# Kernel optimization log

Hardware: AMD Instinct MI355X
Metric: run time of the kernel (lower is better)

Reference implementation:

```python
import jax, jax.numpy as jnp
import numpy as np

V, D, T, L, H = 32000, 1024, 2048, 2, 16
HS = D // H  # per-head dim (head_size // nheads)
FF = 4 * D
EPS = 1e-5


def _ln(x, g, b):
    m = jnp.mean(x, axis=-1, keepdims=True)
    v = jnp.mean((x - m) ** 2, axis=-1, keepdims=True)
    return (x - m) * jax.lax.rsqrt(v + EPS) * g + b


def setup_inputs() -> dict:
    key = jax.random.key(0)
    ks = jax.random.split(key, 16)
    s = lambda k, shape, fan: jax.random.normal(k, shape, jnp.float32) * (fan ** -0.5)
    return {
        "inputs": jax.random.randint(ks[0], (1, T), 0, V, dtype=jnp.int64),
        "tok_emb": s(ks[1], (V, D), D),
        "pos_emb": s(ks[2], (T, D), D),
        "ln1_g": jnp.ones((L, D)), "ln1_b": jnp.zeros((L, D)),
        "wq": s(ks[3], (L, H, D, HS), D),
        "wk": s(ks[4], (L, H, D, HS), D),
        "wv": s(ks[5], (L, H, D, HS), D),
        "ln2_g": jnp.ones((L, D)), "ln2_b": jnp.zeros((L, D)),
        "w1": s(ks[6], (L, D, FF), D), "b1": jnp.zeros((L, FF)),
        "w2": s(ks[7], (L, FF, D), FF), "b2": jnp.zeros((L, D)),
        "lnf_g": jnp.ones((D,)), "lnf_b": jnp.zeros((D,)),
        "w_un": s(ks[8], (D, V), D), "b_un": jnp.zeros((V,)),
    }


def reference(inputs, tok_emb, pos_emb, ln1_g, ln1_b, wq, wk, wv,
              ln2_g, ln2_b, w1, b1, w2, b2, lnf_g, lnf_b, w_un, b_un):
    b, t = inputs.shape
    x = tok_emb[inputs] + pos_emb[:t]  # [B,T,D]
    mask = jnp.tril(jnp.ones((t, t), dtype=bool))
    scale = jnp.asarray(D, x.dtype) ** -0.5  # source scales by x.shape[-1]**-0.5
    neg_inf = jnp.asarray(-jnp.inf, x.dtype)
    for l in range(L):
        h = _ln(x, ln1_g[l], ln1_b[l])
        q = jnp.einsum('btc,hcs->bhts', h, wq[l])
        k = jnp.einsum('btc,hcs->bhts', h, wk[l])
        v = jnp.einsum('btc,hcs->bhts', h, wv[l])
        scores = jnp.einsum('bhts,bhus->bhtu', q, k) * scale  # [B,H,T,T]
        scores = jnp.where(mask, scores, neg_inf)
        p = jax.nn.softmax(scores, axis=-1)
        att = jnp.einsum('bhtu,bhus->bhts', p, v)  # [B,H,T,HS]
        att = att.transpose(0, 2, 1, 3).reshape(b, t, H * HS)
        x = x + att
        h = _ln(x, ln2_g[l], ln2_b[l])
        h = jax.nn.relu(h @ w1[l] + b1[l]) @ w2[l] + b2[l]
        x = x + h
    x = _ln(x, lnf_g, lnf_b)
    return x @ w_un + b_un  # [B,T,V]
```

## Files before the change

### kernel.cpp

```cpp
#include <hip/hip_runtime.h>
#include <hip/hip_bf16.h>

#define TT 2048
#define DD 1024
#define NH 16
#define HSZ 64
#define FFD 4096
#define VV 32000
#define NL 2

typedef __bf16 bf16x8 __attribute__((ext_vector_type(8)));
typedef float f32x4 __attribute__((ext_vector_type(4)));

__device__ __forceinline__ unsigned short f2bf(float f) {
    unsigned int u = __float_as_uint(f);
    return (unsigned short)((u + 0x7FFFu + ((u >> 16) & 1u)) >> 16);
}

#define GLL(gsrc, ldst) \
  __builtin_amdgcn_global_load_lds((const __attribute__((address_space(1))) void*)(gsrc), \
                                   (__attribute__((address_space(3))) void*)(ldst), 16, 0, 0)

#define SWZ64(L)  ((L) ^ ((((L) >> 7) & 3) << 4))
#define SWZ128(L) ((L) ^ ((((L) >> 7) & 7) << 4))

__global__ __launch_bounds__(256) void embed_kernel(
    const int* __restrict__ idx, const float* __restrict__ tok,
    const float* __restrict__ pos, float* __restrict__ x)
{
    int t = blockIdx.x;
    int d4 = threadIdx.x * 4;
    int token = idx[t];
    float4 a = *(const float4*)&tok[(size_t)token * DD + d4];
    float4 p = *(const float4*)&pos[(size_t)t * DD + d4];
    float4 r;
    r.x = a.x + p.x; r.y = a.y + p.y; r.z = a.z + p.z; r.w = a.w + p.w;
    *(float4*)&x[(size_t)t * DD + d4] = r;
}

__global__ __launch_bounds__(256) void ln_kernel(
    const float* __restrict__ x, const float* __restrict__ g,
    const float* __restrict__ b, unsigned short* __restrict__ out)
{
    int t = blockIdx.x;
    int tid = threadIdx.x;
    int d4 = tid * 4;
    float4 xv = *(const float4*)&x[(size_t)t * DD + d4];
    float s  = xv.x + xv.y + xv.z + xv.w;
    float s2 = xv.x*xv.x + xv.y*xv.y + xv.z*xv.z + xv.w*xv.w;
    #pragma unroll
    for (int off = 32; off >= 1; off >>= 1) {
        s  += __shfl_xor(s,  off);
        s2 += __shfl_xor(s2, off);
    }
    __shared__ float ls[4], ls2[4];
    int w = tid >> 6;
    if ((tid & 63) == 0) { ls[w] = s; ls2[w] = s2; }
    __syncthreads();
    float sum  = ls[0] + ls[1] + ls[2] + ls[3];
    float sum2 = ls2[0] + ls2[1] + ls2[2] + ls2[3];
    float mean = sum * (1.0f / DD);
    float var  = sum2 * (1.0f / DD) - mean * mean;
    float r = rsqrtf(var + 1e-5f);
    float4 gv = *(const float4*)&g[d4];
    float4 bv = *(const float4*)&b[d4];
    ushort4 pk;
    pk.x = f2bf((xv.x - mean) * r * gv.x + bv.x);
    pk.y = f2bf((xv.y - mean) * r * gv.y + bv.y);
    pk.z = f2bf((xv.z - mean) * r * gv.z + bv.z);
    pk.w = f2bf((xv.w - mean) * r * gv.w + bv.w);
    *(ushort4*)&out[(size_t)t * DD + d4] = pk;
}

__global__ __launch_bounds__(256) void tcast(
    const float* __restrict__ src, unsigned short* __restrict__ dst,
    int R, int C, size_t sstride, size_t dstride)
{
    __shared__ float tile[64][65];
    const float* s = src + (size_t)blockIdx.z * sstride;
    unsigned short* d = dst + (size_t)blockIdx.z * dstride;
    int c0 = blockIdx.x * 64, r0 = blockIdx.y * 64;
    #pragma unroll
    for (int i = 0; i < 16; ++i) {
        int id = i * 256 + threadIdx.x;
        int rr = id >> 6, cc = id & 63;
        tile[rr][cc] = s[(size_t)(r0 + rr) * C + (c0 + cc)];
    }
    __syncthreads();
    #pragma unroll
    for (int i = 0; i < 16; ++i) {
        int id = i * 256 + threadIdx.x;
        int cc = id >> 6, rr = id & 63;
        d[(size_t)(c0 + cc) * R + (r0 + rr)] = f2bf(tile[rr][cc]);
    }
}

__global__ __launch_bounds__(256) void qkv_tcast(
    const float* __restrict__ wq, const float* __restrict__ wk,
    const float* __restrict__ wv, unsigned short* __restrict__ dst)
{
    __shared__ float tile[64][65];
    int l = blockIdx.z;
    int mat = blockIdx.y >> 4, hh = blockIdx.y & 15;
    const float* s = (mat == 0) ? wq : (mat == 1) ? wk : wv;
    s += (((size_t)l * NH + hh) * DD) * HSZ;
    int r0 = blockIdx.x * 64;
    #pragma unroll
    for (int i = 0; i < 16; ++i) {
        int id = i * 256 + threadIdx.x;
        int rr = id >> 6, cc = id & 63;
        tile[rr][cc] = s[(size_t)(r0 + rr) * HSZ + cc];
    }
    __syncthreads();
    unsigned short* d = dst + (size_t)l * 3072 * DD + ((size_t)mat * DD + hh * HSZ) * DD;
    #pragma unroll
    for (int i = 0; i < 16; ++i) {
        int id = i * 256 + threadIdx.x;
        int cc = id >> 6, rr = id & 63;
        d[(size_t)cc * DD + (r0 + rr)] = f2bf(tile[rr][cc]);
    }
}

template<int EPI>
__global__ __launch_bounds__(256) void mgemm(
    const unsigned short* __restrict__ A, const unsigned short* __restrict__ Bt,
    const float* __restrict__ bias, void* __restrict__ outp,
    int M, int N, int K)
{
    __shared__ unsigned short As[3][128 * 32];
    __shared__ unsigned short Bs[3][128 * 32];
    int tid = threadIdx.x;
    int w = tid >> 6, lane = tid & 63;
    int l15 = lane & 15, l4 = lane >> 4;
    int bm = blockIdx.y * 128, bn = blockIdx.x * 128;
    int wr = (w >> 1) * 64, wc = (w & 1) * 64;

    f32x4 zz = {0.f, 0.f, 0.f, 0.f};
    f32x4 acc[4][4];
    #pragma unroll
    for (int m = 0; m < 4; ++m)
        #pragma unroll
        for (int n = 0; n < 4; ++n) acc[m][n] = zz;

    int t16 = tid * 16;
    int lg = SWZ64(t16);
    int srow = lg >> 6;
    int skel = (lg & 63) >> 1;
    const unsigned short* aS0 = A + (size_t)(bm + srow) * K + skel;
    const unsigned short* aS1 = A + (size_t)(bm + 64 + srow) * K + skel;
    const unsigned short* bS0 = Bt + (size_t)(bn + srow) * K + skel;
    const unsigned short* bS1 = Bt + (size_t)(bn + 64 + srow) * K + skel;

    #define STAGE(t, slot) do { int kk_ = (t) * 32; \
        GLL(aS0 + kk_, (char*)As[slot] + w * 1024); \
        GLL(aS1 + kk_, (char*)As[slot] + 4096 + w * 1024); \
        GLL(bS0 + kk_, (char*)Bs[slot] + w * 1024); \
        GLL(bS1 + kk_, (char*)Bs[slot] + 4096 + w * 1024); } while (0)

    int aoff[4], boff[4];
    #pragma unroll
    for (int m = 0; m < 4; ++m) {
        int la = (wr + m * 16 + l15) * 64 + l4 * 16;
        aoff[m] = SWZ64(la);
        int lb = (wc + m * 16 + l15) * 64 + l4 * 16;
        boff[m] = SWZ64(lb);
    }

    int nt = K >> 5;
    STAGE(0, 0);
    STAGE(1, 1);
    STAGE(2, 2);
    int slot = 0;
    for (int t = 0; t < nt; ++t) {
        if (t + 2 < nt)      asm volatile("s_waitcnt vmcnt(8)" ::: "memory");
        else if (t + 1 < nt) asm volatile("s_waitcnt vmcnt(4)" ::: "memory");
        else                 asm volatile("s_waitcnt vmcnt(0)" ::: "memory");
        __builtin_amdgcn_sched_barrier(0);
        __builtin_amdgcn_s_barrier();
        __builtin_amdgcn_sched_barrier(0);
        bf16x8 af[4], bfr[4];
        #pragma unroll
        for (int m = 0; m < 4; ++m) af[m] = *(const bf16x8*)((const char*)As[slot] + aoff[m]);
        #pragma unroll
        for (int n = 0; n < 4; ++n) bfr[n] = *(const bf16x8*)((const char*)Bs[slot] + boff[n]);
        #pragma unroll
        for (int m = 0; m < 4; ++m)
            #pragma unroll
            for (int n = 0; n < 4; ++n)
                acc[m][n] = __builtin_amdgcn_mfma_f32_16x16x32_bf16(af[m], bfr[n], acc[m][n], 0, 0, 0);
        __builtin_amdgcn_sched_barrier(0);
        __builtin_amdgcn_s_barrier();
        __builtin_amdgcn_sched_barrier(0);
        if (t + 3 < nt) STAGE(t + 3, slot);
        slot = (slot == 2) ? 0 : slot + 1;
    }
    #undef STAGE

    #pragma unroll
    for (int m = 0; m < 4; ++m) {
        int row0 = bm + wr + m * 16 + l4 * 4;
        #pragma unroll
        for (int n = 0; n < 4; ++n) {
            int col = bn + wc + n * 16 + l15;
            f32x4 v = acc[m][n];
            if (EPI == 0) {
                int mat = col >> 10, hh = (col >> 6) & 15, ss = col & 63;
                unsigned short* base = (unsigned short*)outp + (size_t)mat * ((size_t)NH * TT * HSZ);
                if (mat < 2) {
                    #pragma unroll
                    for (int i = 0; i < 4; ++i)
                        base[((size_t)hh * TT + row0 + i) * HSZ + ss] = f2bf(v[i]);
                } else {
                    ushort4 pk;
                    pk.x = f2bf(v[0]); pk.y = f2bf(v[1]); pk.z = f2bf(v[2]); pk.w = f2bf(v[3]);
                    *(ushort4*)&base[((size_t)hh * HSZ + ss) * TT + row0] = pk;
                }
            } else if (EPI == 1) {
                float bb = bias[col];
                unsigned short* o = (unsigned short*)outp;
                #pragma unroll
                for (int i = 0; i < 4; ++i)
                    o[(size_t)(row0 + i) * FFD + col] = f2bf(fmaxf(v[i] + bb, 0.f));
            } else if (EPI == 2) {
                float bb = bias[col];
                float* xx = (float*)outp;
                #pragma unroll
                for (int i = 0; i < 4; ++i)
                    xx[(size_t)(row0 + i) * DD + col] += v[i] + bb;
            }
        }
    }
}

__global__ __launch_bounds__(512, 2) void mgemm256(
    const unsigned short* __restrict__ A, const unsigned short* __restrict__ Bt,
    const float* __restrict__ bias, float* __restrict__ outp,
    int M, int N, int K)
{
    __shared__ unsigned short As[3][2][128 * 32];
    __shared__ unsigned short Bs[3][2][128 * 32];
    int tid = threadIdx.x;
    int w = tid >> 6, lane = tid & 63;
    int l15 = lane & 15, l4 = lane >> 4;
    int wr = w >> 2, wc = w & 3;
    int bid = blockIdx.x;
    int xcd = bid & 7, j = bid >> 3;
    int mt = j & 7, p = xcd * 16 + (j >> 3);
    if (p >= N / 256) return;
    int bm = mt * 256, bn = p * 256;

    f32x4 zz = {0.f, 0.f, 0.f, 0.f};
    f32x4 acc[8][4];
    #pragma unroll
    for (int m = 0; m < 8; ++m)
        #pragma unroll
        for (int n = 0; n < 4; ++n) acc[m][n] = zz;

    int L0 = tid * 16;
    int Ls = SWZ64(L0);
    int srow = Ls >> 6;
    int skel = (Ls & 63) >> 1;
    const unsigned short* aS[2], *bS[2];
    aS[0] = A + (size_t)(bm + srow) * K + skel;
    aS[1] = A + (size_t)(bm + 128 + srow) * K + skel;
    bS[0] = Bt + (size_t)(bn + srow) * K + skel;
    bS[1] = Bt + (size_t)(bn + 128 + srow) * K + skel;

    #define STAGE6(t, slot) do { int kk_ = (t) * 32; \
        GLL(aS[0] + kk_, (char*)As[slot][0] + w * 1024); \
        GLL(aS[1] + kk_, (char*)As[slot][1] + w * 1024); \
        GLL(bS[0] + kk_, (char*)Bs[slot][0] + w * 1024); \
        GLL(bS[1] + kk_, (char*)Bs[slot][1] + w * 1024); } while (0)

    int aoff[8], boff[4];
    #pragma unroll
    for (int m = 0; m < 8; ++m)
        aoff[m] = SWZ64((m * 16 + l15) * 64 + l4 * 16);
    #pragma unroll
    for (int n = 0; n < 4; ++n)
        boff[n] = SWZ64(((wc & 1) * 64 + n * 16 + l15) * 64 + l4 * 16);

    int nt = K >> 5;
    STAGE6(0, 0);
    STAGE6(1, 1);
    STAGE6(2, 2);
    int slot = 0;
    for (int t = 0; t < nt; ++t) {
        if (t + 2 < nt)      asm volatile("s_waitcnt vmcnt(8)" ::: "memory");
        else if (t + 1 < nt) asm volatile("s_waitcnt vmcnt(4)" ::: "memory");
        else                 asm volatile("s_waitcnt vmcnt(0)" ::: "memory");
        __builtin_amdgcn_sched_barrier(0);
        __builtin_amdgcn_s_barrier();
        __builtin_amdgcn_sched_barrier(0);
        const char* ab = (const char*)As[slot][wr];
        const char* bb = (const char*)Bs[slot][wc >> 1];
        bf16x8 bfr[4];
        #pragma unroll
        for (int n = 0; n < 4; ++n) bfr[n] = *(const bf16x8*)(bb + boff[n]);
        __builtin_amdgcn_s_setprio(1);
        #pragma unroll
        for (int m = 0; m < 8; ++m) {
            bf16x8 af = *(const bf16x8*)(ab + aoff[m]);
            #pragma unroll
            for (int n = 0; n < 4; ++n)
                acc[m][n] = __builtin_amdgcn_mfma_f32_16x16x32_bf16(af, bfr[n], acc[m][n], 0, 0, 0);
        }
        __builtin_amdgcn_s_setprio(0);
        __builtin_amdgcn_sched_barrier(0);
        __builtin_amdgcn_s_barrier();
        __builtin_amdgcn_sched_barrier(0);
        if (t + 3 < nt) STAGE6(t + 3, slot);
        slot = (slot == 2) ? 0 : slot + 1;
    }
    #undef STAGE6

    #pragma unroll
    for (int m = 0; m < 8; ++m) {
        int row0 = bm + wr * 128 + m * 16 + l4 * 4;
        #pragma unroll
        for (int n = 0; n < 4; ++n) {
            int col = bn + wc * 64 + n * 16 + l15;
            float bb = bias[col];
            f32x4 v = acc[m][n];
            #pragma unroll
            for (int i = 0; i < 4; ++i)
                outp[(size_t)(row0 + i) * VV + col] = v[i] + bb;
        }
    }
}

__global__ __launch_bounds__(256) void attn_kernel(
    const unsigned short* __restrict__ qg, const unsigned short* __restrict__ kg,
    const unsigned short* __restrict__ vt, float* __restrict__ x)
{
    __shared__ unsigned short Ks[2][64 * 64];
    __shared__ unsigned short Vs[2][64 * 64];
    __shared__ unsigned short Ps[4][16 * 64];
    int tid = threadIdx.x;
    int w = tid >> 6, lane = tid & 63;
    int l15 = lane & 15, l4 = lane >> 4;
    int hh = blockIdx.y;
    int qb = (31 - blockIdx.x) * 64;

    const unsigned short* qrow = qg + ((size_t)hh * TT + qb + w * 16 + l15) * HSZ + l4 * 8;
    bf16x8 qf0 = *(const bf16x8*)(qrow);
    bf16x8 qf1 = *(const bf16x8*)(qrow + 32);

    int t16 = tid * 16;
    int lgs = SWZ128(t16);
    int surow = lgs >> 7;
    int subyte = lgs & 127;
    const char* kbase = (const char*)(kg + (size_t)hh * TT * HSZ);
    const char* vbase = (const char*)(vt + (size_t)hh * HSZ * TT);

    #define ASTAGE(ib, buf) do { \
        int ub_ = (ib) * 64; \
        GLL(kbase + (size_t)(ub_ + surow) * 128 + subyte,          (char*)Ks[buf] + w * 1024); \
        GLL(kbase + (size_t)(ub_ + 32 + surow) * 128 + subyte,     (char*)Ks[buf] + 4096 + w * 1024); \
        GLL(vbase + (size_t)surow * 4096 + ub_ * 2 + subyte,       (char*)Vs[buf] + w * 1024); \
        GLL(vbase + (size_t)(surow + 32) * 4096 + ub_ * 2 + subyte,(char*)Vs[buf] + 4096 + w * 1024); \
    } while (0)

    f32x4 zz = {0.f, 0.f, 0.f, 0.f};
    f32x4 o[4];
    #pragma unroll
    for (int i = 0; i < 4; ++i) o[i] = zz;
    float mrun = -INFINITY, lrun = 0.f;

    const float scale = 0.03125f;
    int nkv = (qb >> 6) + 1;
    ASTAGE(0, 0);
    if (nkv > 1) ASTAGE(1, 1);
    int cur = 0;
    for (int ib = 0; ib < nkv; ++ib) {
        bool diag = (ib * 64 == qb);
        if (ib + 1 < nkv) asm volatile("s_waitcnt vmcnt(4)" ::: "memory");
        else              asm volatile("s_waitcnt vmcnt(0)" ::: "memory");
        __builtin_amdgcn_sched_barrier(0);
        __builtin_amdgcn_s_barrier();
        __builtin_amdgcn_sched_barrier(0);
        const char* ksc = (const char*)Ks[cur];
        const char* vsc = (const char*)Vs[cur];

        f32x4 sfr[4];
        __builtin_amdgcn_s_setprio(1);
        #pragma unroll
        for (int f = 0; f < 4; ++f) {
            int lgb = (f * 16 + l15) * 128 + l4 * 16;
            bf16x8 k0 = *(const bf16x8*)(ksc + SWZ128(lgb));
            bf16x8 k1 = *(const bf16x8*)(ksc + SWZ128(lgb + 64));
            f32x4 z = zz;
            z = __builtin_amdgcn_mfma_f32_16x16x32_bf16(k0, qf0, z, 0, 0, 0);
            z = __builtin_amdgcn_mfma_f32_16x16x32_bf16(k1, qf1, z, 0, 0, 0);
            sfr[f] = z;
        }
        __builtin_amdgcn_s_setprio(0);

        float mx = -INFINITY;
        #pragma unroll
        for (int f = 0; f < 4; ++f)
            #pragma unroll
            for (int i = 0; i < 4; ++i) {
                float s = sfr[f][i] * scale;
                if (diag && (16 * f + (l4 << 2) + i) > (w * 16 + l15)) s = -INFINITY;
                sfr[f][i] = s;
                mx = fmaxf(mx, s);
            }
        mx = fmaxf(mx, __shfl_xor(mx, 16));
        mx = fmaxf(mx, __shfl_xor(mx, 32));
        bool grow = __any(mx > mrun + 8.0f);
        float c = 1.0f;
        if (grow) {
            float mn = fmaxf(mrun, mx);
            c = __expf(mrun - mn);
            mrun = mn;
        }
        float ps = 0.f;
        #pragma unroll
        for (int f = 0; f < 4; ++f)
            #pragma unroll
            for (int i = 0; i < 4; ++i) {
                float p = __expf(sfr[f][i] - mrun);
                sfr[f][i] = p;
                ps += p;
            }
        ps += __shfl_xor(ps, 16);
        ps += __shfl_xor(ps, 32);
        lrun = lrun * c + ps;
        if (grow) {
            #pragma unroll
            for (int i = 0; i < 4; ++i) {
                float ci = __shfl(c, (lane & 48) + (l4 << 2) + i);
                #pragma unroll
                for (int sf = 0; sf < 4; ++sf) o[sf][i] *= ci;
            }
        }

        unsigned short* pw = Ps[w];
        #pragma unroll
        for (int f = 0; f < 4; ++f) {
            unsigned a0 = ((unsigned)f2bf(sfr[f][0])) | (((unsigned)f2bf(sfr[f][1])) << 16);
            unsigned a1 = ((unsigned)f2bf(sfr[f][2])) | (((unsigned)f2bf(sfr[f][3])) << 16);
            int byte0 = l15 * 128 + (16 * f + (l4 << 2)) * 2;
            *(unsigned*)((char*)pw + SWZ128(byte0)) = a0;
            *(unsigned*)((char*)pw + SWZ128(byte0 + 4)) = a1;
        }
        bf16x8 pa0 = *(const bf16x8*)((const char*)pw + SWZ128(l15 * 128 + l4 * 16));
        bf16x8 pa1 = *(const bf16x8*)((const char*)pw + SWZ128(l15 * 128 + 64 + l4 * 16));
        __builtin_amdgcn_s_setprio(1);
        #pragma unroll
        for (int sf = 0; sf < 4; ++sf) {
            int lgb = (sf * 16 + l15) * 128 + l4 * 16;
            bf16x8 v0 = *(const bf16x8*)(vsc + SWZ128(lgb));
            bf16x8 v1 = *(const bf16x8*)(vsc + SWZ128(lgb + 64));
            o[sf] = __builtin_amdgcn_mfma_f32_16x16x32_bf16(pa0, v0, o[sf], 0, 0, 0);
            o[sf] = __builtin_amdgcn_mfma_f32_16x16x32_bf16(pa1, v1, o[sf], 0, 0, 0);
        }
        __builtin_amdgcn_s_setprio(0);
        __builtin_amdgcn_sched_barrier(0);
        __builtin_amdgcn_s_barrier();
        __builtin_amdgcn_sched_barrier(0);
        if (ib + 2 < nkv) ASTAGE(ib + 2, cur);
        cur ^= 1;
    }
    #undef ASTAGE
    float rl[4];
    #pragma unroll
    for (int i = 0; i < 4; ++i)
        rl[i] = 1.0f / __shfl(lrun, (lane & 48) + (l4 << 2) + i);
    #pragma unroll
    for (int sf = 0; sf < 4; ++sf)
        #pragma unroll
        for (int i = 0; i < 4; ++i) {
            int q = qb + w * 16 + l4 * 4 + i;
            int d = hh * HSZ + sf * 16 + l15;
            x[(size_t)q * DD + d] += o[sf][i] * rl[i];
        }
}

extern "C" void kernel_launch(void* const* d_in, const int* in_sizes, int n_in,
                              void* d_out, int out_size, void* d_ws, size_t ws_size,
                              hipStream_t stream)
{
    const int*   idx    = (const int*)  d_in[0];
    const float* tok    = (const float*)d_in[1];
    const float* pos    = (const float*)d_in[2];
    const float* ln1_g  = (const float*)d_in[3];
    const float* ln1_b  = (const float*)d_in[4];
    const float* wq     = (const float*)d_in[5];
    const float* wk     = (const float*)d_in[6];
    const float* wv     = (const float*)d_in[7];
    const float* ln2_g  = (const float*)d_in[8];
    const float* ln2_b  = (const float*)d_in[9];
    const float* w1     = (const float*)d_in[10];
    const float* b1     = (const float*)d_in[11];
    const float* w2     = (const float*)d_in[12];
    const float* b2     = (const float*)d_in[13];
    const float* lnf_g  = (const float*)d_in[14];
    const float* lnf_b  = (const float*)d_in[15];
    const float* w_un   = (const float*)d_in[16];
    const float* b_un   = (const float*)d_in[17];
    float* out = (float*)d_out;

    char* W = (char*)d_ws;
    float*          x    = (float*)(W);
    unsigned short* h    = (unsigned short*)(W + 8388608);
    unsigned short* qg   = (unsigned short*)(W + 12582912);
    unsigned short* kg   = (unsigned short*)(W + 16777216);
    unsigned short* vt   = (unsigned short*)(W + 20971520);
    unsigned short* h1   = (unsigned short*)(W + 25165824);
    unsigned short* wqkvT= (unsigned short*)(W + 41943040);
    unsigned short* w1T  = (unsigned short*)(W + 54525952);
    unsigned short* w2T  = (unsigned short*)(W + 71303168);
    unsigned short* wunT = (unsigned short*)(W + 88080384);
    (void)kg; (void)ws_size; (void)in_sizes; (void)n_in; (void)out_size;

    qkv_tcast<<<dim3(16, 48, 2), 256, 0, stream>>>(wq, wk, wv, wqkvT);
    tcast<<<dim3(64, 16, 2), 256, 0, stream>>>(w1, w1T, DD, FFD, (size_t)DD * FFD, (size_t)DD * FFD);
    tcast<<<dim3(16, 64, 2), 256, 0, stream>>>(w2, w2T, FFD, DD, (size_t)FFD * DD, (size_t)FFD * DD);
    tcast<<<dim3(500, 16, 1), 256, 0, stream>>>(w_un, wunT, DD, VV, 0, 0);

    embed_kernel<<<TT, 256, 0, stream>>>(idx, tok, pos, x);

    for (int l = 0; l < NL; ++l) {
        ln_kernel<<<TT, 256, 0, stream>>>(x, ln1_g + l * DD, ln1_b + l * DD, h);
        mgemm<0><<<dim3(24, 16), 256, 0, stream>>>(h, wqkvT + (size_t)l * 3072 * DD, nullptr, qg, TT, 3072, DD);
        attn_kernel<<<dim3(32, 16), 256, 0, stream>>>(qg, kg, vt, x);
        ln_kernel<<<TT, 256, 0, stream>>>(x, ln2_g + l * DD, ln2_b + l * DD, h);
        mgemm<1><<<dim3(32, 16), 256, 0, stream>>>(h, w1T + (size_t)l * FFD * DD, b1 + (size_t)l * FFD, h1, TT, FFD, DD);
        mgemm<2><<<dim3(8, 16), 256, 0, stream>>>(h1, w2T + (size_t)l * DD * FFD, b2 + (size_t)l * DD, x, TT, DD, FFD);
    }

    ln_kernel<<<TT, 256, 0, stream>>>(x, lnf_g, lnf_b, h);
    mgemm256<<<dim3(1024), 512, 0, stream>>>(h, wunT, b_un, out, TT, VV, DD);
}
```

Baseline: 717.7 us.

## Restructure unembedding GEMM to 256x128 tiles with K=64 two-phase pipelined stages

The final vocabulary GEMM now uses 256x128 output tiles, a K step of 64 with 128-byte swizzled LDS rows, and splits each K step into two half-M phases. Global-to-LDS prefetches for the stage two ahead are interleaved between the LDS fragment reads and the MFMA bursts, with waitcnt and barrier placement chosen by hand. The grid doubles to 2048 blocks so that 250 N tiles can be covered, which adds parallelism and lowers per-thread accumulator registers. The trade-off is more barriers per K step and re-reading A for twice as many N tiles.

```diff
diff --git a/kernel.cpp b/kernel.cpp
--- a/kernel.cpp
+++ b/kernel.cpp
@@ -23,6 +23,8 @@
 
 #define SWZ64(L)  ((L) ^ ((((L) >> 7) & 3) << 4))
 #define SWZ128(L) ((L) ^ ((((L) >> 7) & 7) << 4))
+
+#define VMW(n) asm volatile("s_waitcnt vmcnt(" #n ")" ::: "memory")
 
 __global__ __launch_bounds__(256) void embed_kernel(
     const int* __restrict__ idx, const float* __restrict__ tok,
@@ -172,9 +174,9 @@
     STAGE(2, 2);
     int slot = 0;
     for (int t = 0; t < nt; ++t) {
-        if (t + 2 < nt)      asm volatile("s_waitcnt vmcnt(8)" ::: "memory");
-        else if (t + 1 < nt) asm volatile("s_waitcnt vmcnt(4)" ::: "memory");
-        else                 asm volatile("s_waitcnt vmcnt(0)" ::: "memory");
+        if (t + 2 < nt)      VMW(8);
+        else if (t + 1 < nt) VMW(4);
+        else                 VMW(0);
         __builtin_amdgcn_sched_barrier(0);
         __builtin_amdgcn_s_barrier();
         __builtin_amdgcn_sched_barrier(0);
@@ -237,89 +239,114 @@
     const float* __restrict__ bias, float* __restrict__ outp,
     int M, int N, int K)
 {
-    __shared__ unsigned short As[3][2][128 * 32];
-    __shared__ unsigned short Bs[3][2][128 * 32];
+    __shared__ unsigned short As[3][256 * 64];
+    __shared__ unsigned short Bs[3][128 * 64];
     int tid = threadIdx.x;
     int w = tid >> 6, lane = tid & 63;
     int l15 = lane & 15, l4 = lane >> 4;
     int wr = w >> 2, wc = w & 3;
     int bid = blockIdx.x;
     int xcd = bid & 7, j = bid >> 3;
-    int mt = j & 7, p = xcd * 16 + (j >> 3);
-    if (p >= N / 256) return;
-    int bm = mt * 256, bn = p * 256;
+    int mt = j & 7, pn = xcd * 32 + (j >> 3);
+    if (pn >= N / 128) return;
+    int bm = mt * 256, bn = pn * 128;
 
     f32x4 zz = {0.f, 0.f, 0.f, 0.f};
-    f32x4 acc[8][4];
+    f32x4 acc[8][2];
+    #pragma unroll
+    for (int m = 0; m < 8; ++m) { acc[m][0] = zz; acc[m][1] = zz; }
+
+    int Lw = w * 1024 + lane * 16;
+    int Ls = SWZ128(Lw);
+    int srow = Ls >> 7;
+    int skel = (Ls & 127) >> 1;
+    const unsigned short* aU[4];
+    const unsigned short* bU[2];
+    #pragma unroll
+    for (int u = 0; u < 4; ++u) aU[u] = A + (size_t)(bm + u * 64 + srow) * K + skel;
+    #pragma unroll
+    for (int u = 0; u < 2; ++u) bU[u] = Bt + (size_t)(bn + u * 64 + srow) * K + skel;
+
+    #define SGA(s2, u, kk) GLL(aU[u] + (kk), (char*)As[s2] + (u) * 8192 + w * 1024)
+    #define SGB(s2, u, kk) GLL(bU[u] + (kk), (char*)Bs[s2] + (u) * 8192 + w * 1024)
+
+    int aoff[8][2], boff[2][2];
     #pragma unroll
     for (int m = 0; m < 8; ++m)
         #pragma unroll
-        for (int n = 0; n < 4; ++n) acc[m][n] = zz;
-
-    int L0 = tid * 16;
-    int Ls = SWZ64(L0);
-    int srow = Ls >> 6;
-    int skel = (Ls & 63) >> 1;
-    const unsigned short* aS[2], *bS[2];
-    aS[0] = A + (size_t)(bm + srow) * K + skel;
-    aS[1] = A + (size_t)(bm + 128 + srow) * K + skel;
-    bS[0] = Bt + (size_t)(bn + srow) * K + skel;
-    bS[1] = Bt + (size_t)(bn + 128 + srow) * K + skel;
-
-    #define STAGE6(t, slot) do { int kk_ = (t) * 32; \
-        GLL(aS[0] + kk_, (char*)As[slot][0] + w * 1024); \
-        GLL(aS[1] + kk_, (char*)As[slot][1] + w * 1024); \
-        GLL(bS[0] + kk_, (char*)Bs[slot][0] + w * 1024); \
-        GLL(bS[1] + kk_, (char*)Bs[slot][1] + w * 1024); } while (0)
-
-    int aoff[8], boff[4];
-    #pragma unroll
-    for (int m = 0; m < 8; ++m)
-        aoff[m] = SWZ64((m * 16 + l15) * 64 + l4 * 16);
-    #pragma unroll
-    for (int n = 0; n < 4; ++n)
-        boff[n] = SWZ64(((wc & 1) * 64 + n * 16 + l15) * 64 + l4 * 16);
-
-    int nt = K >> 5;
-    STAGE6(0, 0);
-    STAGE6(1, 1);
-    STAGE6(2, 2);
+        for (int ks = 0; ks < 2; ++ks)
+            aoff[m][ks] = SWZ128((wr * 128 + m * 16 + l15) * 128 + ks * 64 + l4 * 16);
+    #pragma unroll
+    for (int n = 0; n < 2; ++n)
+        #pragma unroll
+        for (int ks = 0; ks < 2; ++ks)
+            boff[n][ks] = SWZ128((wc * 32 + n * 16 + l15) * 128 + ks * 64 + l4 * 16);
+
+    #define PHASE(slot_, MH, s2_, kk2_, ST_, VMN_) do { \
+        const char* ab_ = (const char*)As[slot_]; \
+        const char* bb_ = (const char*)Bs[slot_]; \
+        bf16x8 af_[4][2], bf_[2][2]; \
+        _Pragma("unroll") \
+        for (int mm_ = 0; mm_ < 4; ++mm_) { \
+            af_[mm_][0] = *(const bf16x8*)(ab_ + aoff[(MH) * 4 + mm_][0]); \
+            af_[mm_][1] = *(const bf16x8*)(ab_ + aoff[(MH) * 4 + mm_][1]); } \
+        _Pragma("unroll") \
+        for (int nn_ = 0; nn_ < 2; ++nn_) { \
+            bf_[nn_][0] = *(const bf16x8*)(bb_ + boff[nn_][0]); \
+            bf_[nn_][1] = *(const bf16x8*)(bb_ + boff[nn_][1]); } \
+        if (ST_) { \
+            if ((MH) == 0) { SGA(s2_, 0, kk2_); SGA(s2_, 1, kk2_); SGB(s2_, 0, kk2_); } \
+            else           { SGA(s2_, 2, kk2_); SGA(s2_, 3, kk2_); SGB(s2_, 1, kk2_); } } \
+        __builtin_amdgcn_s_barrier(); \
+        asm volatile("s_waitcnt lgkmcnt(0)" ::: "memory"); \
+        __builtin_amdgcn_sched_barrier(0); \
+        __builtin_amdgcn_s_setprio(1); \
+        _Pragma("unroll") \
+        for (int mm_ = 0; mm_ < 4; ++mm_) \
+            _Pragma("unroll") \
+            for (int nn_ = 0; nn_ < 2; ++nn_) { \
+                acc[(MH) * 4 + mm_][nn_] = __builtin_amdgcn_mfma_f32_16x16x32_bf16(af_[mm_][0], bf_[nn_][0], acc[(MH) * 4 + mm_][nn_], 0, 0, 0); \
+                acc[(MH) * 4 + mm_][nn_] = __builtin_amdgcn_mfma_f32_16x16x32_bf16(af_[mm_][1], bf_[nn_][1], acc[(MH) * 4 + mm_][nn_], 0, 0, 0); } \
+        __builtin_amdgcn_s_setprio(0); \
+        __builtin_amdgcn_sched_barrier(0); \
+        if ((VMN_) == 6) { VMW(6); __builtin_amdgcn_sched_barrier(0); } \
+        else if ((VMN_) == 0) { VMW(0); __builtin_amdgcn_sched_barrier(0); } \
+        __builtin_amdgcn_s_barrier(); \
+        __builtin_amdgcn_sched_barrier(0); \
+    } while (0)
+
+    SGA(0, 0, 0); SGA(0, 1, 0); SGA(0, 2, 0); SGA(0, 3, 0);
+    SGB(0, 0, 0); SGB(0, 1, 0);
+    SGA(1, 0, 64); SGA(1, 1, 64); SGA(1, 2, 64); SGA(1, 3, 64);
+    SGB(1, 0, 64); SGB(1, 1, 64);
+    VMW(6);
+    __builtin_amdgcn_sched_barrier(0);
+    __builtin_amdgcn_s_barrier();
+    __builtin_amdgcn_sched_barrier(0);
+
+    int nt = K >> 6;
     int slot = 0;
+    #pragma unroll 1
     for (int t = 0; t < nt; ++t) {
-        if (t + 2 < nt)      asm volatile("s_waitcnt vmcnt(8)" ::: "memory");
-        else if (t + 1 < nt) asm volatile("s_waitcnt vmcnt(4)" ::: "memory");
-        else                 asm volatile("s_waitcnt vmcnt(0)" ::: "memory");
-        __builtin_amdgcn_sched_barrier(0);
-        __builtin_amdgcn_s_barrier();
-        __builtin_amdgcn_sched_barrier(0);
-        const char* ab = (const char*)As[slot][wr];
-        const char* bb = (const char*)Bs[slot][wc >> 1];
-        bf16x8 bfr[4];
-        #pragma unroll
-        for (int n = 0; n < 4; ++n) bfr[n] = *(const bf16x8*)(bb + boff[n]);
-        __builtin_amdgcn_s_setprio(1);
-        #pragma unroll
-        for (int m = 0; m < 8; ++m) {
-            bf16x8 af = *(const bf16x8*)(ab + aoff[m]);
-            #pragma unroll
-            for (int n = 0; n < 4; ++n)
-                acc[m][n] = __builtin_amdgcn_mfma_f32_16x16x32_bf16(af, bfr[n], acc[m][n], 0, 0, 0);
-        }
-        __builtin_amdgcn_s_setprio(0);
-        __builtin_amdgcn_sched_barrier(0);
-        __builtin_amdgcn_s_barrier();
-        __builtin_amdgcn_sched_barrier(0);
-        if (t + 3 < nt) STAGE6(t + 3, slot);
+        int s2 = slot + 2; if (s2 >= 3) s2 -= 3;
+        int kk2 = (t + 2) << 6;
+        bool st = (t + 2) < nt;
+        PHASE(slot, 0, s2, kk2, st, -1);
+        if (t + 2 < nt)      PHASE(slot, 1, s2, kk2, true,  6);
+        else if (t + 1 < nt) PHASE(slot, 1, s2, kk2, false, 0);
+        else                 PHASE(slot, 1, s2, kk2, false, -1);
         slot = (slot == 2) ? 0 : slot + 1;
     }
-    #undef STAGE6
+    #undef PHASE
+    #undef SGA
+    #undef SGB
 
     #pragma unroll
     for (int m = 0; m < 8; ++m) {
         int row0 = bm + wr * 128 + m * 16 + l4 * 4;
         #pragma unroll
-        for (int n = 0; n < 4; ++n) {
-            int col = bn + wc * 64 + n * 16 + l15;
+        for (int n = 0; n < 2; ++n) {
+            int col = bn + wc * 32 + n * 16 + l15;
             float bb = bias[col];
             f32x4 v = acc[m][n];
             #pragma unroll
@@ -374,8 +401,8 @@
     int cur = 0;
     for (int ib = 0; ib < nkv; ++ib) {
         bool diag = (ib * 64 == qb);
-        if (ib + 1 < nkv) asm volatile("s_waitcnt vmcnt(4)" ::: "memory");
-        else              asm volatile("s_waitcnt vmcnt(0)" ::: "memory");
+        if (ib + 1 < nkv) VMW(4);
+        else              VMW(0);
         __builtin_amdgcn_sched_barrier(0);
         __builtin_amdgcn_s_barrier();
         __builtin_amdgcn_sched_barrier(0);
@@ -532,5 +559,5 @@
     }
 
     ln_kernel<<<TT, 256, 0, stream>>>(x, lnf_g, lnf_b, h);
-    mgemm256<<<dim3(1024), 512, 0, stream>>>(h, wunT, b_un, out, TT, VV, DD);
-}
+    mgemm256<<<dim3(2048), 512, 0, stream>>>(h, wunT, b_un, out, TT, VV, DD);
+}
```

New measurement: 730.0 us. About the same (+1.7%).
